# Kernel tuning notes

Measured on AMD Instinct MI355X. Metric: run time of the kernel, lower is better.

Reference implementation:

```python
import jax, jax.numpy as jnp
import numpy as np

B, C, IMG, P = 8, 3, 64, 8
E, H, BS, L, NC = 256, 2, 8, 128, 10
HD = E // H
N = (IMG // P) ** 2 + 1  # 65 tokens (64 patches + cls)
NEG = -1e30  # stands in for -inf fill of block-diagonal scores
SCALE = float(np.sqrt(HD))


def _ln(x, g, b):
    m = jnp.mean(x, -1, keepdims=True)
    v = jnp.mean((x - m) ** 2, -1, keepdims=True)
    return (x - m) * jax.lax.rsqrt(v + 1e-5) * g + b


def _sparse_attn(x, wq, bq, wk, bk, wv, bv, fp):
    # Block-diagonal attention: only bs x bs diagonal blocks are finite, so we
    # reshape into non-overlapping blocks instead of materializing (B,N,H,N).
    Bx, Nx, Ex = x.shape
    q = (x @ wq + bq).reshape(Bx, Nx, H, HD)
    k = (x @ wk + bk).reshape(Bx, Nx, H, HD)
    v = (x @ wv + bv).reshape(Bx, Nx, H, HD)
    q = jnp.einsum('bnhe,ei->bnhi', q, fp)
    k = jnp.einsum('bnhe,ei->bnhi', k, fp)
    pad = (-Nx) % BS
    Np = Nx + pad
    G = Np // BS
    padf = lambda t: jnp.pad(t, ((0, 0), (0, pad), (0, 0), (0, 0)))
    qb = padf(q).reshape(Bx, G, BS, H, HD)
    kb = padf(k).reshape(Bx, G, BS, H, HD)
    vb = padf(v).reshape(Bx, G, BS, H, HD)
    scores = jnp.einsum('bgqhd,bgkhd->bgqhk', qb, kb) / SCALE  # (B,G,bs,H,bs)
    valid = (jnp.arange(Np) < Nx).reshape(G, BS)  # mask padded keys in last block
    scores = jnp.where(valid[None, :, None, None, :], scores, NEG)
    attn = jax.nn.softmax(scores, axis=-1)
    out = jnp.einsum('bgqhk,bgkhd->bgqhd', attn, vb).reshape(Bx, Np, Ex)
    return out[:, :Nx]


def setup_inputs() -> dict:
    key = jax.random.key(0)
    ks = jax.random.split(key, 12)
    s = 0.02
    f = lambda k, shp: (jax.random.normal(k, shp, jnp.float32) * s)
    z = lambda shp: jnp.zeros(shp, jnp.float32)
    o = lambda shp: jnp.ones(shp, jnp.float32)
    return {
        'src': jax.random.normal(ks[0], (B, C, IMG, IMG), jnp.float32),
        'conv_w': f(ks[1], (E, C, P, P)),
        'conv_b': z((E,)),
        'pos_emb': f(ks[2], (1, N, E)),
        'cls_tok': z((1, 1, E)),
        'Wq': f(ks[3], (L, E, E)), 'bq': z((L, E)),
        'Wk': f(ks[4], (L, E, E)), 'bk': z((L, E)),
        'Wv': f(ks[5], (L, E, E)), 'bv': z((L, E)),
        'fproj': f(ks[6], (L, HD, HD)),
        'ln1_g': o((L, E)), 'ln1_b': z((L, E)),
        'ln2_g': o((L, E)), 'ln2_b': z((L, E)),
        'ff1_w': f(ks[7], (L, E, 4 * E)), 'ff1_b': z((L, 4 * E)),
        'ff2_w': f(ks[8], (L, 4 * E, E)), 'ff2_b': z((L, E)),
        'fc_w': f(ks[9], (E, NC)), 'fc_b': z((NC,)),
    }


def reference(src, conv_w, conv_b, pos_emb, cls_tok, Wq, bq, Wk, bk, Wv, bv,
              fproj, ln1_g, ln1_b, ln2_g, ln2_b, ff1_w, ff1_b, ff2_w, ff2_b,
              fc_w, fc_b):
    # patch embedding (Conv2d stride=patch) -> flatten(2).transpose(1,2)
    x = jax.lax.conv_general_dilated(
        src, conv_w, (P, P), 'VALID',
        dimension_numbers=('NCHW', 'OIHW', 'NCHW')) + conv_b[None, :, None, None]
    x = x.reshape(B, E, -1).transpose(0, 2, 1)  # (B, num_patches, E)
    x = jnp.concatenate([jnp.broadcast_to(cls_tok, (B, 1, E)), x], axis=1)
    x = x + pos_emb

    params = (Wq, bq, Wk, bk, Wv, bv, fproj, ln1_g, ln1_b, ln2_g, ln2_b,
              ff1_w, ff1_b, ff2_w, ff2_b)

    def enc(h, p):
        wq, bq_, wk, bk_, wv, bv_, fp, g1, b1, g2, b2, w1, bb1, w2, bb2 = p
        h = h + _sparse_attn(_ln(h, g1, b1), wq, bq_, wk, bk_, wv, bv_, fp)
        hn = _ln(h, g2, b2)
        hf = jax.nn.gelu(hn @ w1 + bb1, approximate=False)  # dropout = eval identity
        h = h + hf @ w2 + bb2
        return h, None

    x, _ = jax.lax.scan(enc, x, params)
    return x[:, 0] @ fc_w + fc_b
```

## Files before the change

kernel.cpp:

```cpp
#include <hip/hip_runtime.h>
#include <math.h>

typedef __attribute__((ext_vector_type(8))) short short8v;
typedef __attribute__((ext_vector_type(4))) float float4v;

#if defined(__has_builtin)
#if __has_builtin(__builtin_amdgcn_global_load_lds)
#define USE_GLL 1
#endif
#endif
#ifndef USE_GLL
#define USE_GLL 0
#endif

__device__ __forceinline__ float gelu_f(float v) {
    return 0.5f * v * (1.0f + erff(v * 0.70710678118654752440f));
}

__device__ __forceinline__ unsigned short bf16r(float f) {
    unsigned u = __float_as_uint(f);
    u += 0x7FFFu + ((u >> 16) & 1u);
    return (unsigned short)(u >> 16);
}

__device__ __forceinline__ float bf2f(unsigned short s) {
    return __uint_as_float(((unsigned)s) << 16);
}

__global__ void dump_k(float* __restrict__ out, int n, float val) {
    int t = blockIdx.x * 256 + threadIdx.x;
    if (t < n) out[t] = val;
}

__global__ void tc_k(const float* __restrict__ in0, unsigned short* __restrict__ out0,
                     int R, int Cc, long long ils, long long ols) {
    __shared__ float tile[32][33];
    int l = blockIdx.z;
    const float* in = in0 + (size_t)l * ils;
    unsigned short* out = out0 + (size_t)l * ols;
    int t = threadIdx.x;
    int tx = t & 31, ty = t >> 5;
    int r0 = blockIdx.x * 32, c0 = blockIdx.y * 32;
#pragma unroll
    for (int i = 0; i < 4; ++i) {
        int r = r0 + ty + i * 8, c = c0 + tx;
        tile[ty + i * 8][tx] = (r < R && c < Cc) ? in[(size_t)r * Cc + c] : 0.f;
    }
    __syncthreads();
#pragma unroll
    for (int i = 0; i < 4; ++i) {
        int c = c0 + ty + i * 8, r = r0 + tx;
        if (c < Cc && r < R) out[(size_t)c * R + r] = bf16r(tile[tx][ty + i * 8]);
    }
}

__global__ void fold_k(const float* __restrict__ Wq0, const float* __restrict__ Wk0,
                       const float* __restrict__ fp0, unsigned short* __restrict__ Wt0,
                       int E, int HD, int mode) {
    extern __shared__ float fpS[];
    int l = blockIdx.z;
    long long EE = (long long)E * E;
    const float* fp = fp0 + (size_t)l * HD * HD;
    unsigned short* Wt = Wt0 + (size_t)l * 3 * EE;
    int t = threadIdx.x;
    int n0 = blockIdx.x * 64;
    int n = n0 + (t & 63);
    int cg = t >> 6;

    int i0 = 0;
    if (mode == 0) {
        for (int idx = t; idx < HD * HD; idx += 256) fpS[idx] = fp[idx];
    } else if (mode == 1) {
        int base = (n0 < E) ? n0 : n0 - E;
        i0 = base % HD;
        for (int idx = t; idx < HD * 64; idx += 256)
            fpS[idx] = fp[(size_t)(idx >> 6) * HD + i0 + (idx & 63)];
    }
    __syncthreads();
    if (n >= 2 * E) return;
    int s = (n >= E) ? 1 : 0;
    int idd = n - s * E;
    int h = idd / HD, i = idd % HD;
    const float* W = (s ? Wk0 : Wq0) + (size_t)l * EE;
    for (int c = cg; c < E; c += 4) {
        const float* Wr = W + (size_t)c * E + h * HD;
        float acc = 0.f;
        if (mode == 0) {
            for (int d = 0; d < HD; ++d) acc += Wr[d] * fpS[d * HD + i];
        } else if (mode == 1) {
            for (int d = 0; d < HD; ++d) acc += Wr[d] * fpS[d * 64 + (i - i0)];
        } else {
            for (int d = 0; d < HD; ++d) acc += Wr[d] * fp[(size_t)d * HD + i];
        }
        Wt[(size_t)n * E + c] = bf16r(acc);
    }
}

__global__ void biasfold_k(const float* __restrict__ bq0, const float* __restrict__ bk0,
                           const float* __restrict__ bv0, const float* __restrict__ fp0,
                           float* __restrict__ bqkv0, int E, int HD) {
    int l = blockIdx.z;
    const float* bq = bq0 + (size_t)l * E;
    const float* bk = bk0 + (size_t)l * E;
    const float* bv = bv0 + (size_t)l * E;
    const float* fp = fp0 + (size_t)l * HD * HD;
    float* bqkv = bqkv0 + (size_t)l * 3 * E;
    int c = blockIdx.x * 256 + threadIdx.x;
    if (c >= 3 * E) return;
    if (c < 2 * E) {
        int mat = c / E, cc = c % E, h = cc / HD, j = cc % HD;
        const float* bb = mat ? bk : bq;
        float s = 0.f;
        for (int d = 0; d < HD; ++d) s += bb[h * HD + d] * fp[(size_t)d * HD + j];
        bqkv[c] = s;
    } else {
        bqkv[c] = bv[c - 2 * E];
    }
}

__global__ __launch_bounds__(512) void gemm2_k(
        const unsigned short* __restrict__ A, int lda,
        const unsigned short* __restrict__ Bt, int ldbt,
        void* __restrict__ Cv, int ldc,
        const float* __restrict__ bias,
        int M, int Nn, int K, int op, int al) {
    __shared__ unsigned short Ab[128 * 64];
    __shared__ unsigned short Bb[128 * 64];
    int t = threadIdx.x;
    int m0 = blockIdx.x * 128, n0 = blockIdx.y * 128;
    int w = t >> 6, lane = t & 63;
    int wm = w >> 2, wn = w & 3;
    int lrow = lane & 15, lk = lane >> 4;

    float4v acc[4][2];
#pragma unroll
    for (int fa = 0; fa < 4; ++fa)
#pragma unroll
        for (int fb = 0; fb < 2; ++fb) acc[fa][fb] = (float4v){0.f, 0.f, 0.f, 0.f};

    int srow8 = lane >> 3;
    int sch = lane & 7;
    bool fastA = al && (m0 + 128 <= M);
    bool fastB = al && (n0 + 128 <= Nn);

    for (int k0 = 0; k0 < K; k0 += 64) {
        bool fullK = (k0 + 64 <= K);
        __syncthreads();
#if USE_GLL
        if (fastA && fullK) {
#pragma unroll
            for (int it = 0; it < 2; ++it) {
                int r = w * 16 + it * 8 + srow8;
                const unsigned short* g = A + (size_t)(m0 + r) * lda + k0 + ((sch ^ (r & 7)) << 3);
                __builtin_amdgcn_global_load_lds((const void*)g, (void*)&Ab[(w * 16 + it * 8) * 64], 16, 0, 0);
            }
        } else
#endif
        {
#pragma unroll
            for (int cc = 0; cc < 2; ++cc) {
                int c = t + cc * 512;
                int row = c >> 3, ch = c & 7;
                int gm = m0 + row, gk = k0 + ch * 8;
                short8v v = {0, 0, 0, 0, 0, 0, 0, 0};
                if (gm < M) {
                    if (al && gk + 8 <= K) {
                        v = *(const short8v*)(A + (size_t)gm * lda + gk);
                    } else {
                        const unsigned short* p = A + (size_t)gm * lda;
#pragma unroll
                        for (int j = 0; j < 8; ++j)
                            if (gk + j < K) v[j] = (short)p[gk + j];
                    }
                }
                *(short8v*)&Ab[row * 64 + ((ch ^ (row & 7)) << 3)] = v;
            }
        }
#if USE_GLL
        if (fastB && fullK) {
#pragma unroll
            for (int it = 0; it < 2; ++it) {
                int r = w * 16 + it * 8 + srow8;
                const unsigned short* g = Bt + (size_t)(n0 + r) * ldbt + k0 + ((sch ^ (r & 7)) << 3);
                __builtin_amdgcn_global_load_lds((const void*)g, (void*)&Bb[(w * 16 + it * 8) * 64], 16, 0, 0);
            }
        } else
#endif
        {
#pragma unroll
            for (int cc = 0; cc < 2; ++cc) {
                int c = t + cc * 512;
                int row = c >> 3, ch = c & 7;
                int gn = n0 + row, gk = k0 + ch * 8;
                short8v v = {0, 0, 0, 0, 0, 0, 0, 0};
                if (gn < Nn) {
                    if (al && gk + 8 <= K) {
                        v = *(const short8v*)(Bt + (size_t)gn * ldbt + gk);
                    } else {
                        const unsigned short* p = Bt + (size_t)gn * ldbt;
#pragma unroll
                        for (int j = 0; j < 8; ++j)
                            if (gk + j < K) v[j] = (short)p[gk + j];
                    }
                }
                *(short8v*)&Bb[row * 64 + ((ch ^ (row & 7)) << 3)] = v;
            }
        }
        __syncthreads();
#pragma unroll
        for (int ks = 0; ks < 2; ++ks) {
            short8v af[4], bf[2];
#pragma unroll
            for (int fa = 0; fa < 4; ++fa) {
                int row = wm * 64 + fa * 16 + lrow;
                af[fa] = *(const short8v*)&Ab[row * 64 + (((ks * 4 + lk) ^ (row & 7)) << 3)];
            }
#pragma unroll
            for (int fb = 0; fb < 2; ++fb) {
                int row = wn * 32 + fb * 16 + lrow;
                bf[fb] = *(const short8v*)&Bb[row * 64 + (((ks * 4 + lk) ^ (row & 7)) << 3)];
            }
#pragma unroll
            for (int fa = 0; fa < 4; ++fa)
#pragma unroll
                for (int fb = 0; fb < 2; ++fb)
                    acc[fa][fb] = __builtin_amdgcn_mfma_f32_16x16x32_bf16(
                        af[fa], bf[fb], acc[fa][fb], 0, 0, 0);
        }
    }
    float* Cf = (float*)Cv;
    unsigned short* Cu = (unsigned short*)Cv;
#pragma unroll
    for (int fb = 0; fb < 2; ++fb) {
        int col = n0 + wn * 32 + fb * 16 + lrow;
        if (col >= Nn) continue;
        float bb = bias ? bias[col] : 0.f;
#pragma unroll
        for (int fa = 0; fa < 4; ++fa) {
#pragma unroll
            for (int q = 0; q < 4; ++q) {
                int row = m0 + wm * 64 + fa * 16 + lk * 4 + q;
                if (row >= M) continue;
                float v = acc[fa][fb][q] + bb;
                size_t idx = (size_t)row * ldc + col;
                if (op == 0) Cf[idx] = v;
                else if (op == 1) Cu[idx] = bf16r(gelu_f(v));
                else if (op == 2) Cf[idx] += v;
                else Cu[idx] = bf16r(v);
            }
        }
    }
}

__global__ void embed_lds_k(const float* __restrict__ src, const float* __restrict__ cw,
                            const float* __restrict__ cb, const float* __restrict__ pos,
                            const float* __restrict__ cls, float* __restrict__ x,
                            int C, int IMG, int P, int m, int E, int N, int K) {
    extern __shared__ float patch[];
    int n = blockIdx.x, b = blockIdx.y, t = threadIdx.x;
    if (n == 0) {
        for (int e = t; e < E; e += 256)
            x[((size_t)b * N) * E + e] = cls[e] + pos[e];
        return;
    }
    int p = n - 1, ph = p / m, pw = p % m;
    int P2 = P * P;
    for (int mm = t; mm < K; mm += 256) {
        int c = mm / P2, rem = mm % P2, i = rem / P, j = rem % P;
        patch[mm] = src[(((size_t)b * C + c) * IMG + ph * P + i) * IMG + pw * P + j];
    }
    __syncthreads();
    for (int e = t; e < E; e += 256) {
        float acc = cb[e];
        const float* wr = cw + (size_t)e * K;
        for (int mm = 0; mm < K; ++mm) acc += patch[mm] * wr[mm];
        x[((size_t)b * N + n) * E + e] = acc + pos[(size_t)n * E + e];
    }
}

__global__ void embed_dir_k(const float* __restrict__ src, const float* __restrict__ cw,
                            const float* __restrict__ cb, const float* __restrict__ pos,
                            const float* __restrict__ cls, float* __restrict__ x,
                            int C, int IMG, int P, int m, int E, int N, int K) {
    int n = blockIdx.x, b = blockIdx.y, t = threadIdx.x;
    if (n == 0) {
        for (int e = t; e < E; e += 256)
            x[((size_t)b * N) * E + e] = cls[e] + pos[e];
        return;
    }
    int p = n - 1, ph = p / m, pw = p % m;
    int P2 = P * P;
    for (int e = t; e < E; e += 256) {
        float acc = cb[e];
        const float* wr = cw + (size_t)e * K;
        for (int mm = 0; mm < K; ++mm) {
            int c = mm / P2, rem = mm % P2, i = rem / P, j = rem % P;
            acc += src[(((size_t)b * C + c) * IMG + ph * P + i) * IMG + pw * P + j] * wr[mm];
        }
        x[((size_t)b * N + n) * E + e] = acc + pos[(size_t)n * E + e];
    }
}

__global__ void ln_k(const float* __restrict__ x, const float* __restrict__ g,
                     const float* __restrict__ b, unsigned short* __restrict__ xg,
                     int TOK, int E, float invE) {
    int row = blockIdx.x * 4 + (threadIdx.x >> 6);
    int lane = threadIdx.x & 63;
    if (row >= TOK) return;
    const float* xr = x + (size_t)row * E;
    float s = 0.f;
    for (int e = lane; e < E; e += 64) s += xr[e];
#pragma unroll
    for (int mm = 32; mm >= 1; mm >>= 1) s += __shfl_xor(s, mm, 64);
    float mean = s * invE;
    float v = 0.f;
    for (int e = lane; e < E; e += 64) { float d = xr[e] - mean; v += d * d; }
#pragma unroll
    for (int mm = 32; mm >= 1; mm >>= 1) v += __shfl_xor(v, mm, 64);
    float inv = rsqrtf(v * invE + 1e-5f);
    unsigned short* orow = xg + (size_t)row * E;
    for (int e = lane; e < E; e += 64)
        orow[e] = bf16r((xr[e] - mean) * inv * g[e] + b[e]);
}

__global__ void attn_sm_k(const unsigned short* __restrict__ qkv, float* __restrict__ x,
                          int img0, int N, int E, int H, int HD, float rscale, int vec) {
    extern __shared__ float sc[];
    int g = blockIdx.x, im = blockIdx.y, t = threadIdx.x;
    int t0 = g * 8, nv = min(8, N - t0);
    int E3 = 3 * E;
    const unsigned short* qb = qkv + ((size_t)im * N + t0) * E3;
    float* xb = x + (((size_t)(img0 + im)) * N + t0) * E;
    for (int idx = t; idx < H * 64; idx += 256) {
        int h = idx >> 6, qr = (idx >> 3) & 7, kr = idx & 7;
        float s = 0.f;
        if (qr < nv && kr < nv) {
            const unsigned short* qp = qb + (size_t)qr * E3 + h * HD;
            const unsigned short* kp = qb + (size_t)kr * E3 + E + h * HD;
            if (vec) {
                for (int d = 0; d < HD; d += 8) {
                    short8v qv = *(const short8v*)(qp + d);
                    short8v kv = *(const short8v*)(kp + d);
#pragma unroll
                    for (int j = 0; j < 8; ++j)
                        s += bf2f((unsigned short)qv[j]) * bf2f((unsigned short)kv[j]);
                }
            } else {
                for (int d = 0; d < HD; ++d)
                    s += bf2f(qp[d]) * bf2f(kp[d]);
            }
        }
        sc[idx] = s * rscale;
    }
    __syncthreads();
    for (int idx = t; idx < H * 8; idx += 256) {
        int h = idx >> 3, qr = idx & 7;
        if (qr < nv) {
            float* row = sc + h * 64 + qr * 8;
            float mx = -1e30f;
            for (int k = 0; k < nv; ++k) mx = fmaxf(mx, row[k]);
            float sum = 0.f;
            for (int k = 0; k < nv; ++k) { float e = expf(row[k] - mx); row[k] = e; sum += e; }
            float inv = 1.f / sum;
            for (int k = 0; k < nv; ++k) row[k] *= inv;
        }
    }
    __syncthreads();
    for (int c = t; c < E; c += 256) {
        int h = c / HD;
        const float* srow = sc + h * 64;
        float vcol[8];
#pragma unroll
        for (int k = 0; k < 8; ++k)
            vcol[k] = (k < nv) ? bf2f(qb[(size_t)k * E3 + 2 * E + c]) : 0.f;
        for (int r = 0; r < nv; ++r) {
            float o = 0.f;
#pragma unroll
            for (int k = 0; k < 8; ++k) o += srow[r * 8 + k] * vcol[k];
            xb[(size_t)r * E + c] += o;
        }
    }
}

__global__ void head_k(const float* __restrict__ fw, const float* __restrict__ fb,
                       const float* __restrict__ x, float* __restrict__ out,
                       int Bc, int N, int E, int NC) {
    int idx = blockIdx.x * 256 + threadIdx.x;
    if (idx < Bc * NC) {
        int b = idx / NC, nc = idx % NC;
        float acc = fb[nc];
        const float* xr = x + (size_t)b * N * E;
        for (int e = 0; e < E; ++e) acc += xr[e] * fw[(size_t)e * NC + nc];
        out[idx] = acc;
    }
}

static int isqrt_i(long long v) {
    if (v < 0) return -1;
    long long r = (long long)(sqrt((double)v) + 0.5);
    while (r * r > v) --r;
    while ((r + 1) * (r + 1) <= v) ++r;
    return (int)r;
}

extern "C" void kernel_launch(void* const* d_in, const int* in_sizes, int n_in,
                              void* d_out, int out_size, void* d_ws, size_t ws_size,
                              hipStream_t stream) {
    float* out = (float*)d_out;
    int nblk_out = (out_size + 255) / 256;
#define DUMP(code, val) do { \
        dump_k<<<nblk_out, 256, 0, stream>>>(out, out_size, (float)((code) * 1000000.0 + (double)(val))); \
        return; } while (0)

    if (n_in != 22) DUMP(1, n_in < 999999 ? n_in : 999999);
    const int* S = in_sizes;

    int E = S[2];
    if (E <= 0 || S[4] != E) DUMP(2, 4);
    if (S[6] % E) DUMP(2, 6);
    int L = S[6] / E;
    if (L <= 0) DUMP(2, 6);
    long long EE = (long long)E * E;
    if (S[5] != L * EE || S[7] != L * EE || S[9] != L * EE) DUMP(2, 5);
    if (S[8] != L * E || S[10] != L * E) DUMP(2, 8);
    if (S[12] != L * E || S[13] != L * E || S[14] != L * E || S[15] != L * E) DUMP(2, 12);
    if (S[19] != L * E) DUMP(2, 19);
    if (S[11] % L) DUMP(2, 11);
    int HD = isqrt_i(S[11] / L);
    if ((long long)HD * HD * L != S[11] || HD <= 0 || E % HD) DUMP(3, HD > 0 ? HD : 0);
    int H = E / HD;
    if (S[17] % L) DUMP(2, 17);
    int FF = S[17] / L;
    if (S[16] != (long long)L * E * FF) DUMP(2, 16);
    if (S[18] != (long long)L * FF * E) DUMP(2, 18);
    if (S[3] % E) DUMP(2, 3);
    int N = S[3] / E;
    int m = isqrt_i(N - 1);
    if (m <= 0 || m * m != N - 1) DUMP(4, N < 999999 ? N : 999999);
    int NC = S[21];
    if (NC <= 0 || S[20] != (long long)E * NC) DUMP(2, 20);
    if (out_size % NC) DUMP(8, out_size < 999999 ? out_size : 999999);
    int Bc = out_size / NC;
    if (S[1] % E) DUMP(2, 1);
    int K = S[1] / E;
    static const int corder[12] = {3, 4, 1, 2, 8, 16, 6, 12, 32, 64, 24, 48};
    int C = -1, P = -1;
    for (int ci = 0; ci < 12; ++ci) {
        int c = corder[ci];
        if (K % c) continue;
        int p = isqrt_i(K / c);
        if (p > 0 && p * p * c == K) {
            long long img = (long long)p * m;
            if ((long long)Bc * c * img * img == S[0]) { C = c; P = p; break; }
        }
    }
    if (C < 0) DUMP(5, K < 999999 ? K : 999999);
    int IMG = P * m;
    int TOK = Bc * N;
    int Gg = (N + 7) / 8;
    int E3 = 3 * E;
    int al = ((E % 8) == 0 && (FF % 8) == 0) ? 1 : 0;
    int vecA = (al && (HD % 8) == 0) ? 1 : 0;

    int fmode;
    if (HD <= 64) fmode = 0;
    else if ((E % 64) == 0 && HD <= 256) fmode = 1;
    else fmode = 2;
    size_t fold_sh = (fmode == 0) ? (size_t)HD * HD * 4
                   : (fmode == 1) ? (size_t)HD * 64 * 4 : 16;

    size_t b_x  = ((size_t)TOK * E * 4 + 255) & ~(size_t)255;
    size_t b_xg = ((size_t)TOK * E * 2 + 255) & ~(size_t)255;
    size_t s_wt  = ((size_t)E3 * E * 2 + 255) & ~(size_t)255;
    size_t s_wff = ((size_t)E * FF * 2 + 255) & ~(size_t)255;
    size_t s_bq  = ((size_t)E3 * 4 + 255) & ~(size_t)255;
    size_t perL = s_wt + 2 * s_wff + s_bq;
    size_t minbuf = (size_t)N * E3 * 2;
    size_t fb2 = (size_t)128 * FF * 2;
    if (fb2 > minbuf) minbuf = fb2;

    int LW;
    if (b_x + b_xg + perL * L + minbuf <= ws_size) LW = L;
    else if (b_x + b_xg + perL + minbuf <= ws_size) LW = 1;
    else { DUMP(6, (double)(ws_size >> 20)); }

    char* wsb = (char*)d_ws;
    size_t off = 0;
    float* x = (float*)(wsb + off); off += b_x;
    unsigned short* xg = (unsigned short*)(wsb + off); off += b_xg;
    unsigned short* Wt_base = (unsigned short*)(wsb + off); off += s_wt * LW;
    unsigned short* w1t_base = (unsigned short*)(wsb + off); off += s_wff * LW;
    unsigned short* w2t_base = (unsigned short*)(wsb + off); off += s_wff * LW;
    float* bq_base = (float*)(wsb + off); off += s_bq * LW;
    size_t buf_bytes = ws_size - off;
    unsigned short* bufu = (unsigned short*)(wsb + off);

    int CHI = (int)(buf_bytes / ((size_t)N * E3 * 2));
    if (CHI > Bc) CHI = Bc;
    long long chf_l = (long long)(buf_bytes / ((size_t)FF * 2));
    chf_l = (chf_l / 128) * 128;
    int CHF = chf_l > TOK ? TOK : (int)chf_l;
    if (CHI < 1 || CHF < 128) DUMP(6, (double)(ws_size >> 20));

    const float* src = (const float*)d_in[0];
    const float* cw  = (const float*)d_in[1];
    const float* cb  = (const float*)d_in[2];
    const float* pos = (const float*)d_in[3];
    const float* cls = (const float*)d_in[4];
    const float* Wq  = (const float*)d_in[5];
    const float* bq  = (const float*)d_in[6];
    const float* Wk  = (const float*)d_in[7];
    const float* bk  = (const float*)d_in[8];
    const float* Wv  = (const float*)d_in[9];
    const float* bv  = (const float*)d_in[10];
    const float* fp  = (const float*)d_in[11];
    const float* g1  = (const float*)d_in[12];
    const float* b1  = (const float*)d_in[13];
    const float* g2  = (const float*)d_in[14];
    const float* b2  = (const float*)d_in[15];
    const float* w1  = (const float*)d_in[16];
    const float* bb1 = (const float*)d_in[17];
    const float* w2  = (const float*)d_in[18];
    const float* bb2 = (const float*)d_in[19];
    const float* fcw = (const float*)d_in[20];
    const float* fcb = (const float*)d_in[21];

    float invE = 1.f / (float)E;
    float rscale = 1.f / sqrtf((float)HD);
    size_t wtL = (size_t)E3 * E;
    size_t wffL = (size_t)E * FF;

    size_t patch_sh = (size_t)K * sizeof(float);
    if (patch_sh <= 48000)
        embed_lds_k<<<dim3(N, Bc), 256, patch_sh, stream>>>(src, cw, cb, pos, cls, x,
                                                            C, IMG, P, m, E, N, K);
    else
        embed_dir_k<<<dim3(N, Bc), 256, 0, stream>>>(src, cw, cb, pos, cls, x,
                                                     C, IMG, P, m, E, N, K);

    int gx_fold = (2 * E + 63) / 64;
    if (LW == L) {
        fold_k<<<dim3(gx_fold, 1, L), 256, fold_sh, stream>>>(Wq, Wk, fp, Wt_base, E, HD, fmode);
        tc_k<<<dim3((E + 31) / 32, (E + 31) / 32, L), 256, 0, stream>>>(
            Wv, Wt_base + (size_t)2 * E * E, E, E, EE, wtL);
        tc_k<<<dim3((E + 31) / 32, (FF + 31) / 32, L), 256, 0, stream>>>(
            w1, w1t_base, E, FF, (long long)E * FF, wffL);
        tc_k<<<dim3((FF + 31) / 32, (E + 31) / 32, L), 256, 0, stream>>>(
            w2, w2t_base, FF, E, (long long)E * FF, wffL);
        biasfold_k<<<dim3((E3 + 255) / 256, 1, L), 256, 0, stream>>>(
            bq, bk, bv, fp, bq_base, E, HD);
    }

    int ln_grid = (TOK + 3) / 4;
    size_t attn_sh = (size_t)H * 64 * sizeof(float);

    for (int l = 0; l < L; ++l) {
        int lw = (LW == L) ? l : 0;
        unsigned short* Wt_l  = Wt_base + (size_t)lw * (s_wt / 2);
        unsigned short* w1t_l = w1t_base + (size_t)lw * (s_wff / 2);
        unsigned short* w2t_l = w2t_base + (size_t)lw * (s_wff / 2);
        float* bq_l = (float*)((char*)bq_base + (size_t)lw * s_bq);
        (void)wtL; (void)wffL;

        if (LW != L) {
            fold_k<<<dim3(gx_fold, 1, 1), 256, fold_sh, stream>>>(
                Wq + (size_t)l * EE, Wk + (size_t)l * EE, fp + (size_t)l * HD * HD,
                Wt_l, E, HD, fmode);
            tc_k<<<dim3((E + 31) / 32, (E + 31) / 32, 1), 256, 0, stream>>>(
                Wv + (size_t)l * EE, Wt_l + (size_t)2 * E * E, E, E, 0, 0);
            tc_k<<<dim3((E + 31) / 32, (FF + 31) / 32, 1), 256, 0, stream>>>(
                w1 + (size_t)l * E * FF, w1t_l, E, FF, 0, 0);
            tc_k<<<dim3((FF + 31) / 32, (E + 31) / 32, 1), 256, 0, stream>>>(
                w2 + (size_t)l * FF * E, w2t_l, FF, E, 0, 0);
            biasfold_k<<<dim3((E3 + 255) / 256, 1, 1), 256, 0, stream>>>(
                bq + (size_t)l * E, bk + (size_t)l * E, bv + (size_t)l * E,
                fp + (size_t)l * HD * HD, bq_l, E, HD);
        }

        ln_k<<<ln_grid, 256, 0, stream>>>(x, g1 + (size_t)l * E, b1 + (size_t)l * E,
                                          xg, TOK, E, invE);
        for (int img0 = 0; img0 < Bc; img0 += CHI) {
            int nimg = Bc - img0 < CHI ? Bc - img0 : CHI;
            int ntok = nimg * N;
            gemm2_k<<<dim3((ntok + 127) / 128, (E3 + 127) / 128), 512, 0, stream>>>(
                xg + (size_t)img0 * N * E, E, Wt_l, E, bufu, E3, bq_l,
                ntok, E3, E, 3, al);
            attn_sm_k<<<dim3(Gg, nimg), 256, attn_sh, stream>>>(
                bufu, x, img0, N, E, H, HD, rscale, vecA);
        }
        ln_k<<<ln_grid, 256, 0, stream>>>(x, g2 + (size_t)l * E, b2 + (size_t)l * E,
                                          xg, TOK, E, invE);
        for (int tok0 = 0; tok0 < TOK; tok0 += CHF) {
            int ntok = TOK - tok0 < CHF ? TOK - tok0 : CHF;
            int gx = (ntok + 127) / 128;
            gemm2_k<<<dim3(gx, (FF + 127) / 128), 512, 0, stream>>>(
                xg + (size_t)tok0 * E, E, w1t_l, E, bufu, FF,
                bb1 + (size_t)l * FF, ntok, FF, E, 1, al);
            gemm2_k<<<dim3(gx, (E + 127) / 128), 512, 0, stream>>>(
                bufu, FF, w2t_l, FF, x + (size_t)tok0 * E, E,
                bb2 + (size_t)l * E, ntok, E, FF, 2, al);
        }
    }
    head_k<<<nblk_out, 256, 0, stream>>>(fcw, fcb, x, out, Bc, N, E, NC);
#undef DUMP
}
```

Before: 10.21 ms.

## Fuse second LayerNorm into attention kernel and remap GEMM tiles across XCDs

The second LayerNorm of each layer now runs at the end of the attention kernel, on the 8 rows each block just updated. This removes one kernel launch per layer and one extra read of the activations. Separately, the GEMM grid is flattened to 1D and block IDs are remapped so consecutive tiles land on the same XCD, aiming for better L2 locality. The fused LN relies on each block's rows being final after its own attention update, which holds because each block owns its 8-token group.

```diff
diff --git a/kernel.cpp b/kernel.cpp
--- a/kernel.cpp
+++ b/kernel.cpp
@@ -123,11 +123,16 @@
         const unsigned short* __restrict__ Bt, int ldbt,
         void* __restrict__ Cv, int ldc,
         const float* __restrict__ bias,
-        int M, int Nn, int K, int op, int al) {
+        int M, int Nn, int K, int op, int al, int nNt) {
     __shared__ unsigned short Ab[128 * 64];
     __shared__ unsigned short Bb[128 * 64];
     int t = threadIdx.x;
-    int m0 = blockIdx.x * 128, n0 = blockIdx.y * 128;
+    int nwg = gridDim.x;
+    int orig = blockIdx.x;
+    int xcd = orig & 7, pos = orig >> 3;
+    int q = nwg >> 3, r = nwg & 7;
+    int wgid = (xcd < r ? xcd * (q + 1) : r * (q + 1) + (xcd - r) * q) + pos;
+    int m0 = (wgid / nNt) * 128, n0 = (wgid % nNt) * 128;
     int w = t >> 6, lane = t & 63;
     int wm = w >> 2, wn = w & 3;
     int lrow = lane & 15, lk = lane >> 4;
@@ -150,8 +155,8 @@
         if (fastA && fullK) {
 #pragma unroll
             for (int it = 0; it < 2; ++it) {
-                int r = w * 16 + it * 8 + srow8;
-                const unsigned short* g = A + (size_t)(m0 + r) * lda + k0 + ((sch ^ (r & 7)) << 3);
+                int rr = w * 16 + it * 8 + srow8;
+                const unsigned short* g = A + (size_t)(m0 + rr) * lda + k0 + ((sch ^ (rr & 7)) << 3);
                 __builtin_amdgcn_global_load_lds((const void*)g, (void*)&Ab[(w * 16 + it * 8) * 64], 16, 0, 0);
             }
         } else
@@ -180,8 +185,8 @@
         if (fastB && fullK) {
 #pragma unroll
             for (int it = 0; it < 2; ++it) {
-                int r = w * 16 + it * 8 + srow8;
-                const unsigned short* g = Bt + (size_t)(n0 + r) * ldbt + k0 + ((sch ^ (r & 7)) << 3);
+                int rr = w * 16 + it * 8 + srow8;
+                const unsigned short* g = Bt + (size_t)(n0 + rr) * ldbt + k0 + ((sch ^ (rr & 7)) << 3);
                 __builtin_amdgcn_global_load_lds((const void*)g, (void*)&Bb[(w * 16 + it * 8) * 64], 16, 0, 0);
             }
         } else
@@ -238,10 +243,10 @@
 #pragma unroll
         for (int fa = 0; fa < 4; ++fa) {
 #pragma unroll
-            for (int q = 0; q < 4; ++q) {
-                int row = m0 + wm * 64 + fa * 16 + lk * 4 + q;
+            for (int q2 = 0; q2 < 4; ++q2) {
+                int row = m0 + wm * 64 + fa * 16 + lk * 4 + q2;
                 if (row >= M) continue;
-                float v = acc[fa][fb][q] + bb;
+                float v = acc[fa][fb][q2] + bb;
                 size_t idx = (size_t)row * ldc + col;
                 if (op == 0) Cf[idx] = v;
                 else if (op == 1) Cu[idx] = bf16r(gelu_f(v));
@@ -324,13 +329,17 @@
 }
 
 __global__ void attn_sm_k(const unsigned short* __restrict__ qkv, float* __restrict__ x,
-                          int img0, int N, int E, int H, int HD, float rscale, int vec) {
+                          unsigned short* __restrict__ xg,
+                          const float* __restrict__ g2, const float* __restrict__ b2,
+                          int img0, int N, int E, int H, int HD, float rscale,
+                          float invE, int vec) {
     extern __shared__ float sc[];
     int g = blockIdx.x, im = blockIdx.y, t = threadIdx.x;
     int t0 = g * 8, nv = min(8, N - t0);
     int E3 = 3 * E;
     const unsigned short* qb = qkv + ((size_t)im * N + t0) * E3;
-    float* xb = x + (((size_t)(img0 + im)) * N + t0) * E;
+    size_t rowbase = ((size_t)(img0 + im)) * N + t0;
+    float* xb = x + rowbase * E;
     for (int idx = t; idx < H * 64; idx += 256) {
         int h = idx >> 6, qr = (idx >> 3) & 7, kr = idx & 7;
         float s = 0.f;
@@ -379,6 +388,27 @@
             for (int k = 0; k < 8; ++k) o += srow[r * 8 + k] * vcol[k];
             xb[(size_t)r * E + c] += o;
         }
+    }
+    __syncthreads();
+    int w = t >> 6, lane = t & 63;
+#pragma unroll
+    for (int rr = 0; rr < 2; ++rr) {
+        int r = w + rr * 4;
+        if (r >= nv) continue;
+        const float* xr = xb + (size_t)r * E;
+        float s = 0.f;
+        for (int e = lane; e < E; e += 64) s += xr[e];
+#pragma unroll
+        for (int mm = 32; mm >= 1; mm >>= 1) s += __shfl_xor(s, mm, 64);
+        float mean = s * invE;
+        float v = 0.f;
+        for (int e = lane; e < E; e += 64) { float d = xr[e] - mean; v += d * d; }
+#pragma unroll
+        for (int mm = 32; mm >= 1; mm >>= 1) v += __shfl_xor(v, mm, 64);
+        float inv = rsqrtf(v * invE + 1e-5f);
+        unsigned short* orow = xg + (rowbase + r) * E;
+        for (int e = lane; e < E; e += 64)
+            orow[e] = bf16r((xr[e] - mean) * inv * g2[e] + b2[e]);
     }
 }
 
@@ -560,7 +590,6 @@
         unsigned short* w1t_l = w1t_base + (size_t)lw * (s_wff / 2);
         unsigned short* w2t_l = w2t_base + (size_t)lw * (s_wff / 2);
         float* bq_l = (float*)((char*)bq_base + (size_t)lw * s_bq);
-        (void)wtL; (void)wffL;
 
         if (LW != L) {
             fold_k<<<dim3(gx_fold, 1, 1), 256, fold_sh, stream>>>(
@@ -582,23 +611,24 @@
         for (int img0 = 0; img0 < Bc; img0 += CHI) {
             int nimg = Bc - img0 < CHI ? Bc - img0 : CHI;
             int ntok = nimg * N;
-            gemm2_k<<<dim3((ntok + 127) / 128, (E3 + 127) / 128), 512, 0, stream>>>(
+            int nMt = (ntok + 127) / 128, nNt = (E3 + 127) / 128;
+            gemm2_k<<<nMt * nNt, 512, 0, stream>>>(
                 xg + (size_t)img0 * N * E, E, Wt_l, E, bufu, E3, bq_l,
-                ntok, E3, E, 3, al);
+                ntok, E3, E, 3, al, nNt);
             attn_sm_k<<<dim3(Gg, nimg), 256, attn_sh, stream>>>(
-                bufu, x, img0, N, E, H, HD, rscale, vecA);
-        }
-        ln_k<<<ln_grid, 256, 0, stream>>>(x, g2 + (size_t)l * E, b2 + (size_t)l * E,
-                                          xg, TOK, E, invE);
+                bufu, x, xg, g2 + (size_t)l * E, b2 + (size_t)l * E,
+                img0, N, E, H, HD, rscale, invE, vecA);
+        }
         for (int tok0 = 0; tok0 < TOK; tok0 += CHF) {
             int ntok = TOK - tok0 < CHF ? TOK - tok0 : CHF;
-            int gx = (ntok + 127) / 128;
-            gemm2_k<<<dim3(gx, (FF + 127) / 128), 512, 0, stream>>>(
+            int nMt = (ntok + 127) / 128;
+            int nNt1 = (FF + 127) / 128, nNt2 = (E + 127) / 128;
+            gemm2_k<<<nMt * nNt1, 512, 0, stream>>>(
                 xg + (size_t)tok0 * E, E, w1t_l, E, bufu, FF,
-                bb1 + (size_t)l * FF, ntok, FF, E, 1, al);
-            gemm2_k<<<dim3(gx, (E + 127) / 128), 512, 0, stream>>>(
+                bb1 + (size_t)l * FF, ntok, FF, E, 1, al, nNt1);
+            gemm2_k<<<nMt * nNt2, 512, 0, stream>>>(
                 bufu, FF, w2t_l, FF, x + (size_t)tok0 * E, E,
-                bb2 + (size_t)l * E, ntok, E, FF, 2, al);
+                bb2 + (size_t)l * E, ntok, E, FF, 2, al, nNt2);
         }
     }
     head_k<<<nblk_out, 256, 0, stream>>>(fcw, fcb, x, out, Bc, N, E, NC);
```

After: 10.15 ms. Within noise of the previous version (-0.6%).
